# Optimization experiments

Measured on AMD Instinct MI355X. Metric: run time of the kernel, lower is better.

## Reference

```python
import jax, jax.numpy as jnp
import numpy as np

B, V, H, NT, K_CD = 4096, 1024, 1024, 2, 10
L1_REG, L2_REG = 1e-5, 1e-4


def setup_inputs() -> dict:
    key = jax.random.key(0)
    ks = jax.random.split(key, 10)
    v0 = jax.random.bernoulli(ks[0], 0.5, (B, V)).astype(jnp.float32)
    # two distinct non-trivial (non-Z) sites per sample, one in each half
    tau0 = jax.random.randint(ks[1], (B,), 0, V // 2)
    tau1 = V // 2 + jax.random.randint(ks[2], (B,), 0, V // 2)
    tau_idx = jnp.stack([tau0, tau1], axis=1).astype(jnp.int32)
    basis_choice = jax.random.randint(ks[3], (B, NT), 1, 3).astype(jnp.int32)  # X=1 or Y=2
    basis_ids = jnp.zeros((B, V), jnp.int32)
    basis_ids = basis_ids.at[jnp.arange(B)[:, None], tau_idx].set(basis_choice)
    s = 1.0 / np.sqrt(2.0)
    un = np.zeros((3, 2, 2, 2), np.float32)  # [basis, row, col, re/im]
    un[0, :, :, 0] = np.eye(2)                              # Z: identity
    un[1, :, :, 0] = s * np.array([[1, 1], [1, -1]])        # X: Hadamard
    un[2, :, :, 0] = s * np.array([[1, 0], [1, 0]])         # Y: K gate, real
    un[2, :, :, 1] = s * np.array([[0, -1], [0, 1]])        # Y: K gate, imag
    unitaries = jnp.asarray(un)
    weights_amp = jax.random.normal(ks[4], (H, V), jnp.float32) / np.sqrt(V)
    weights_phase = 0.01 * jax.random.normal(ks[5], (H, V), jnp.float32)
    visible_bias_amp = 0.01 * jax.random.normal(ks[6], (V,), jnp.float32)
    hidden_bias_amp = 0.01 * jax.random.normal(ks[7], (H,), jnp.float32)
    visible_bias_phase = 0.01 * jax.random.normal(ks[8], (V,), jnp.float32)
    hidden_bias_phase = 0.01 * jax.random.normal(ks[9], (H,), jnp.float32)
    return {"v0": v0, "basis_ids": basis_ids, "tau_idx": tau_idx, "unitaries": unitaries,
            "weights_amp": weights_amp, "visible_bias_amp": visible_bias_amp,
            "hidden_bias_amp": hidden_bias_amp, "weights_phase": weights_phase,
            "visible_bias_phase": visible_bias_phase, "hidden_bias_phase": hidden_bias_phase,
            "k": K_CD}


def _forward(v0, unitaries, weights_amp, visible_bias_amp, hidden_bias_amp,
             weights_phase, visible_bias_phase, hidden_bias_phase,
             basis_ids, tau_idx, k):
    Bsz, Vn = v0.shape
    NTn = tau_idx.shape[1]
    C = 2 ** NTn
    # all 2^NT assignments of the rotated (tau) sites -> [C, NT]
    S = jnp.asarray(np.array([[(c >> (NTn - 1 - t)) & 1 for t in range(NTn)]
                              for c in range(C)], np.int32))
    U = (unitaries[..., 0] + 1j * unitaries[..., 1]).astype(jnp.complex64)  # [3,2,2]
    b_tau = jnp.take_along_axis(basis_ids, tau_idx, axis=1)                 # [B,NT]
    v0_tau = jnp.take_along_axis(v0, tau_idx, axis=1).astype(jnp.int32)     # [B,NT]
    # product over tau sites of unitary elements U_b[v0_j, s_j] -> [B,C]
    Uelem = U[b_tau[:, None, :], v0_tau[:, None, :], S[None, :, :]]
    wU = jnp.prod(Uelem, axis=-1)
    # v' = v0 with tau sites replaced by each assignment s -> [B,C,V]
    onehot = jax.nn.one_hot(tau_idx, Vn, dtype=v0.dtype)                    # [B,NT,V]
    mask = onehot.sum(1)
    vp = v0[:, None, :] * (1.0 - mask[:, None, :]) \
         + jnp.einsum('btv,ct->bcv', onehot, S.astype(v0.dtype))
    # unnormalized wavefunction psi(v') = sqrt(p_amp(v')) * exp(i*log(p_phase(v'))/2)
    pre_amp = jnp.einsum('bcv,hv->bch', vp, weights_amp) + hidden_bias_amp
    pre_ph = jnp.einsum('bcv,hv->bch', vp, weights_phase) + hidden_bias_phase
    log_amp = 0.5 * (vp @ visible_bias_amp + jax.nn.softplus(pre_amp).sum(-1))  # [B,C]
    theta = 0.5 * (vp @ visible_bias_phase + jax.nn.softplus(pre_ph).sum(-1))
    # per-sample shift cancels exactly in A/B; keeps exp() in fp32 range
    log_amp = log_amp - jax.lax.stop_gradient(log_amp.max(axis=1, keepdims=True))
    psi = (jnp.exp(log_amp) * (jnp.cos(theta) + 1j * jnp.sin(theta))).astype(jnp.complex64)
    w = wU * psi                                   # [B,C] complex
    coef = w / w.sum(axis=1, keepdims=True)        # A/B weighting per sample
    sig_amp = jax.nn.sigmoid(pre_amp)
    sig_ph = jax.nn.sigmoid(pre_ph)
    inv_b = 1.0 / Bsz
    Lw_amp = jnp.einsum('bc,bch,bcv->hv', coef, sig_amp, vp) * inv_b
    Lw_ph = jnp.einsum('bc,bch,bcv->hv', coef, sig_ph, vp) * inv_b
    Lvb = jnp.einsum('bc,bcv->v', coef, vp) * inv_b
    Lhb_amp = jnp.einsum('bc,bch->h', coef, sig_amp) * inv_b
    Lhb_ph = jnp.einsum('bc,bch->h', coef, sig_ph) * inv_b
    # amplitude params take Re(L) (negated positive phase); phase params take Im(L)
    g_w_amp = -jnp.real(Lw_amp)
    g_vb_amp = -jnp.real(Lvb)
    g_hb_amp = -jnp.real(Lhb_amp)
    g_w_ph = jnp.imag(Lw_ph)
    g_vb_ph = jnp.imag(Lvb)
    g_hb_ph = jnp.imag(Lhb_ph)
    # ---- CD-k Gibbs negative phase (amplitude RBM only) ----
    base_key = jax.random.key(1234)
    def gibbs_step(i, v):
        kh = jax.random.fold_in(base_key, 2 * i)
        kv = jax.random.fold_in(base_key, 2 * i + 1)
        ph = jax.nn.sigmoid(v @ weights_amp.T + hidden_bias_amp)
        h = (jax.random.uniform(kh, ph.shape) < ph).astype(v.dtype)
        pv = jax.nn.sigmoid(h @ weights_amp + visible_bias_amp)
        return (jax.random.uniform(kv, pv.shape) < pv).astype(v.dtype)
    vk = jax.lax.stop_gradient(jax.lax.fori_loop(0, k, gibbs_step, v0))
    sig_k = jax.nn.sigmoid(vk @ weights_amp.T + hidden_bias_amp)
    g_w_amp = g_w_amp + jnp.einsum('bh,bv->hv', sig_k, vk) * inv_b
    g_vb_amp = g_vb_amp + vk.mean(0)
    g_hb_amp = g_hb_amp + sig_k.mean(0)
    # ---- L1/L2 regularization on weight gradients ----
    g_w_amp = g_w_amp + L2_REG * weights_amp + L1_REG * jnp.sign(weights_amp)
    g_w_ph = g_w_ph + L2_REG * weights_phase + L1_REG * jnp.sign(weights_phase)
    return (g_w_amp, g_vb_amp, g_hb_amp, g_w_ph, g_vb_ph, g_hb_ph)


def reference(v0, basis_ids, tau_idx, unitaries, weights_amp, visible_bias_amp,
              hidden_bias_amp, weights_phase, visible_bias_phase, hidden_bias_phase, k):
    return _forward(v0, unitaries, weights_amp, visible_bias_amp, hidden_bias_amp,
                    weights_phase, visible_bias_phase, hidden_bias_phase,
                    basis_ids, tau_idx, k)
```

## Files before the change

### kernel.cpp

```cpp
#include <hip/hip_runtime.h>
#include <cstdint>
#include <cstddef>

#define BSZ 4096
#define VN  1024
#define HN  1024
#define NSTEPS 10

static constexpr float INVB = 1.0f / 4096.0f;
static constexpr float L1R  = 1e-5f;
static constexpr float L2R  = 1e-4f;

typedef __attribute__((ext_vector_type(8)))  __bf16        bf16x8;
typedef __attribute__((ext_vector_type(8)))  unsigned short ushort8;
typedef __attribute__((ext_vector_type(16))) float          f32x16;

__device__ static inline unsigned short f2bf(float x){
  unsigned u = __float_as_uint(x);
  unsigned r = (u + 0x7FFFu + ((u >> 16) & 1u)) >> 16;
  return (unsigned short)r;
}
__device__ static inline float bf2f(unsigned short s){
  return __uint_as_float(((unsigned)s) << 16);
}

__device__ __forceinline__ void gload16(const void* g, void* l){
  __builtin_amdgcn_global_load_lds(
      (__attribute__((address_space(1))) void*)(g),
      (__attribute__((address_space(3))) void*)(l),
      16, 0, 0);
}

#define TFR(x0,x1,r) { x0 += x1; x1 = ((x1)<<(r))|((x1)>>(32-(r))); x1 ^= x0; }

__host__ __device__ static inline void tf2x32(unsigned k0, unsigned k1,
                                              unsigned x0, unsigned x1,
                                              unsigned &o0, unsigned &o1)
{
  const unsigned ks2 = k0 ^ k1 ^ 0x1BD11BDAu;
  x0 += k0; x1 += k1;
  TFR(x0,x1,13) TFR(x0,x1,15) TFR(x0,x1,26) TFR(x0,x1,6)
  x0 += k1; x1 += ks2 + 1u;
  TFR(x0,x1,17) TFR(x0,x1,29) TFR(x0,x1,16) TFR(x0,x1,24)
  x0 += ks2; x1 += k0 + 2u;
  TFR(x0,x1,13) TFR(x0,x1,15) TFR(x0,x1,26) TFR(x0,x1,6)
  x0 += k0; x1 += k1 + 3u;
  TFR(x0,x1,17) TFR(x0,x1,29) TFR(x0,x1,16) TFR(x0,x1,24)
  x0 += k1; x1 += ks2 + 4u;
  TFR(x0,x1,13) TFR(x0,x1,15) TFR(x0,x1,26) TFR(x0,x1,6)
  x0 += ks2; x1 += k0 + 5u;
  o0 = x0; o1 = x1;
}

__device__ static inline float tf_uniform(unsigned k0, unsigned k1, unsigned e)
{
  unsigned o0, o1; tf2x32(k0, k1, 0u, e, o0, o1);
  const unsigned r = o0 ^ o1;
  return __uint_as_float((r >> 9) | 0x3f800000u) - 1.0f;
}

__device__ static inline float sigmoidf(float x){ return 1.0f/(1.0f+expf(-x)); }
__device__ static inline float softplusf(float x){
  return fmaxf(x, 0.0f) + log1pf(expf(-fabsf(x)));
}

__global__ void zero_kernel(float* __restrict__ p, int n){
  int i = blockIdx.x*256 + threadIdx.x;
  if (i < n) p[i] = 0.0f;
}

__global__ void prep_kernel(const float* __restrict__ v0,
                            const int* __restrict__ tau,
                            float* __restrict__ v0m,
                            float* __restrict__ v_cur,
                            unsigned short* __restrict__ v0m_bf,
                            unsigned short* __restrict__ v_bf)
{
  int i = blockIdx.x*256 + threadIdx.x;
  int b = i >> 10;
  int v = i & (VN-1);
  float x = v0[i];
  v_cur[i] = x;
  v_bf[i]  = f2bf(x);
  int t0 = tau[2*b], t1 = tau[2*b+1];
  float xm = (v==t0 || v==t1) ? 0.0f : x;
  v0m[i]    = xm;
  v0m_bf[i] = f2bf(xm);
}

__global__ void transpose_kernel(const float* __restrict__ Wa,
                                 const float* __restrict__ Wp,
                                 float* __restrict__ WTa,
                                 float* __restrict__ WTp)
{
  __shared__ float tile[32][33];
  const float* in = blockIdx.z ? Wp : Wa;
  float* out      = blockIdx.z ? WTp : WTa;
  int x  = blockIdx.x*32 + threadIdx.x;
  int y0 = blockIdx.y*32;
  for (int j = threadIdx.y; j < 32; j += 8)
    tile[j][threadIdx.x] = in[(size_t)(y0+j)*VN + x];
  __syncthreads();
  int xo  = y0 + threadIdx.x;
  int yo0 = blockIdx.x*32;
  for (int j = threadIdx.y; j < 32; j += 8)
    out[(size_t)(yo0+j)*HN + xo] = tile[threadIdx.x][j];
}

__global__ void transpose_to_bf(const float* __restrict__ X,
                                unsigned short* __restrict__ XT)
{
  __shared__ float tile[32][33];
  int x  = blockIdx.x*32 + threadIdx.x;
  int y0 = blockIdx.y*32;
  for (int j = threadIdx.y; j < 32; j += 8)
    tile[j][threadIdx.x] = X[(size_t)(y0+j)*1024 + x];
  __syncthreads();
  int xo  = y0 + threadIdx.x;
  int yo0 = blockIdx.x*32;
  for (int j = threadIdx.y; j < 32; j += 8)
    XT[(size_t)(yo0+j)*BSZ + xo] = f2bf(tile[threadIdx.x][j]);
}

__global__ void split_weights(const float* __restrict__ Wa,
                              const float* __restrict__ Wp,
                              const float* __restrict__ WTa,
                              unsigned short* __restrict__ WaHi,
                              unsigned short* __restrict__ WaLo,
                              unsigned short* __restrict__ WpHi,
                              unsigned short* __restrict__ WpLo,
                              unsigned short* __restrict__ WaTHi,
                              unsigned short* __restrict__ WaTLo)
{
  size_t i = (size_t)blockIdx.x*256 + threadIdx.x;
  float w = Wa[i];  unsigned short h = f2bf(w);
  WaHi[i] = h;  WaLo[i] = f2bf(w - bf2f(h));
  w = Wp[i];  h = f2bf(w);
  WpHi[i] = h;  WpLo[i] = f2bf(w - bf2f(h));
  w = WTa[i]; h = f2bf(w);
  WaTHi[i] = h; WaTLo[i] = f2bf(w - bf2f(h));
}

#define GM 128
#define GN 64
#define GK 64

template<int MODE>
__global__ __launch_bounds__(256) void mfma_nt(
    const unsigned short* __restrict__ A,
    const unsigned short* __restrict__ Bhi,
    const unsigned short* __restrict__ Blo,
    const float* __restrict__ bias,
    unsigned short* __restrict__ out_bf,
    float* __restrict__ out_f,
    unsigned key0, unsigned key1)
{
  constexpr int K = 1024;
  constexpr int N = 1024;
  __shared__ ushort8 ldsA [GM*8];
  __shared__ ushort8 ldsBh[GN*8];
  __shared__ ushort8 ldsBl[GN*8];

  const int tid  = threadIdx.x;
  const int m0   = blockIdx.y*GM, n0 = blockIdx.x*GN;
  const int lane = tid & 63, w = tid >> 6;
  const int wm = w >> 1, wn = w & 1;
  const int l31 = lane & 31, hi = lane >> 5;

  const int rsub = lane >> 3;
  const int cch  = lane & 7;

  f32x16 acc0 = {}, acc1 = {};

  const int arow0 = wm*64 + l31;
  const int brow  = wn*32 + l31;
  const int aidx0 = arow0*8, aidx1 = (arow0+32)*8;
  const int bidx  = brow*8;
  const int aswz  = arow0 & 7;
  const int bswz  = brow & 7;

  for (int kt = 0; kt < K/GK; ++kt){
    __syncthreads();
    const size_t kbase = (size_t)kt*GK;
    #pragma unroll
    for (int p = 0; p < 4; p++){
      const int row  = p*32 + w*8 + rsub;
      const int csrc = cch ^ (row & 7);
      gload16(A + (size_t)(m0+row)*K + kbase + csrc*8,
              &ldsA[(p*32 + w*8)*8]);
    }
    #pragma unroll
    for (int p = 0; p < 2; p++){
      const int row  = p*32 + w*8 + rsub;
      const int csrc = cch ^ (row & 7);
      gload16(Bhi + (size_t)(n0+row)*K + kbase + csrc*8,
              &ldsBh[(p*32 + w*8)*8]);
      gload16(Blo + (size_t)(n0+row)*K + kbase + csrc*8,
              &ldsBl[(p*32 + w*8)*8]);
    }
    __syncthreads();

    #pragma unroll
    for (int s = 0; s < 4; s++){
      const int c = s*2 + hi;
      const bf16x8 a0 = __builtin_bit_cast(bf16x8, ldsA [aidx0 + (c ^ aswz)]);
      const bf16x8 a1 = __builtin_bit_cast(bf16x8, ldsA [aidx1 + (c ^ aswz)]);
      const bf16x8 bh = __builtin_bit_cast(bf16x8, ldsBh[bidx  + (c ^ bswz)]);
      const bf16x8 bl = __builtin_bit_cast(bf16x8, ldsBl[bidx  + (c ^ bswz)]);
      acc0 = __builtin_amdgcn_mfma_f32_32x32x16_bf16(a0, bh, acc0, 0, 0, 0);
      acc0 = __builtin_amdgcn_mfma_f32_32x32x16_bf16(a0, bl, acc0, 0, 0, 0);
      acc1 = __builtin_amdgcn_mfma_f32_32x32x16_bf16(a1, bh, acc1, 0, 0, 0);
      acc1 = __builtin_amdgcn_mfma_f32_32x32x16_bf16(a1, bl, acc1, 0, 0, 0);
    }
  }

  const int n  = n0 + wn*32 + l31;
  const float bv = bias[n];
  #pragma unroll
  for (int mt = 0; mt < 2; mt++){
    const f32x16 acc = mt ? acc1 : acc0;
    const int mbase = m0 + wm*64 + mt*32 + 4*hi;
    #pragma unroll
    for (int r = 0; r < 16; r++){
      const int m = mbase + (r&3) + 8*(r>>2);
      const float pre = acc[r] + bv;
      const size_t o = (size_t)m*N + n;
      if constexpr (MODE == 0 || MODE == 1){
        const float p = sigmoidf(pre);
        const float u = tf_uniform(key0, key1, (unsigned)(m*N + n));
        const float smp = (u < p) ? 1.0f : 0.0f;
        out_bf[o] = (u < p) ? (unsigned short)0x3F80 : (unsigned short)0;
        if constexpr (MODE == 1) out_f[o] = smp;
      } else if constexpr (MODE == 2){
        out_f[o] = sigmoidf(pre);
      } else {
        out_f[o] = pre;
      }
    }
  }
}

template<int NPROD>
__global__ __launch_bounds__(256) void mfma_grad(
    const unsigned short* __restrict__ A1,
    const unsigned short* __restrict__ B1,
    const unsigned short* __restrict__ A2,
    const unsigned short* __restrict__ B2,
    const float* __restrict__ Wreg,
    float* __restrict__ gW)
{
  constexpr int K = BSZ;
  __shared__ ushort8 lA1[64*8];
  __shared__ ushort8 lB1[64*8];
  __shared__ ushort8 lA2[(NPROD==2)?64*8:1];
  __shared__ ushort8 lB2[(NPROD==2)?64*8:1];

  const int tid  = threadIdx.x;
  const int m0   = blockIdx.y*64, n0 = blockIdx.x*64;
  const int lane = tid & 63, w = tid >> 6;
  const int wm = w >> 1, wn = w & 1;
  const int l31 = lane & 31, hi = lane >> 5;
  const int srow = tid >> 3, sc = tid & 7;

  f32x16 acc1a = {}, acc1b = {}, acc2a = {}, acc2b = {};

  const int arow = wm*32 + l31;
  const int brow = wn*32 + l31;
  const int aswz = arow & 7, bswz = brow & 7;
  const int aidx = arow*8,  bidx = brow*8;

  for (int kt = 0; kt < K/64; ++kt){
    __syncthreads();
    const size_t kof = (size_t)kt*64 + sc*8;
    #pragma unroll
    for (int p = 0; p < 2; p++){
      const int row = p*32 + srow;
      const int c = sc ^ (row & 7);
      lA1[row*8 + c] = *(const ushort8*)(A1 + (size_t)(m0+row)*K + kof);
      lB1[row*8 + c] = *(const ushort8*)(B1 + (size_t)(n0+row)*K + kof);
      if constexpr (NPROD==2){
        lA2[row*8 + c] = *(const ushort8*)(A2 + (size_t)(m0+row)*K + kof);
        lB2[row*8 + c] = *(const ushort8*)(B2 + (size_t)(n0+row)*K + kof);
      }
    }
    __syncthreads();
    #pragma unroll
    for (int s = 0; s < 4; s++){
      const int c = s*2 + hi;
      const bf16x8 a1 = __builtin_bit_cast(bf16x8, lA1[aidx + (c ^ aswz)]);
      const bf16x8 b1 = __builtin_bit_cast(bf16x8, lB1[bidx + (c ^ bswz)]);
      if (s & 1) acc1b = __builtin_amdgcn_mfma_f32_32x32x16_bf16(a1, b1, acc1b, 0,0,0);
      else       acc1a = __builtin_amdgcn_mfma_f32_32x32x16_bf16(a1, b1, acc1a, 0,0,0);
      if constexpr (NPROD==2){
        const bf16x8 a2 = __builtin_bit_cast(bf16x8, lA2[aidx + (c ^ aswz)]);
        const bf16x8 b2 = __builtin_bit_cast(bf16x8, lB2[bidx + (c ^ bswz)]);
        if (s & 1) acc2b = __builtin_amdgcn_mfma_f32_32x32x16_bf16(a2, b2, acc2b, 0,0,0);
        else       acc2a = __builtin_amdgcn_mfma_f32_32x32x16_bf16(a2, b2, acc2a, 0,0,0);
      }
    }
  }

  const int n = n0 + wn*32 + l31;
  #pragma unroll
  for (int r = 0; r < 16; r++){
    const int m = m0 + wm*32 + 4*hi + (r&3) + 8*(r>>2);
    const size_t o = (size_t)m*VN + n;
    float val;
    if constexpr (NPROD==2)
      val = INVB*((acc1a[r]+acc1b[r]) - (acc2a[r]+acc2b[r]));
    else
      val = INVB*(acc1a[r]+acc1b[r]);
    const float wv = Wreg[o];
    const float sg = (wv>0.f)?1.f:((wv<0.f)?-1.f:0.f);
    gW[o] += val + L2R*wv + L1R*sg;
  }
}

__global__ __launch_bounds__(256) void coef_ramp_kernel(
    const float* __restrict__ pre0a, const float* __restrict__ pre0p,
    const float* __restrict__ WTa,   const float* __restrict__ WTp,
    const float* __restrict__ v0,
    const float* __restrict__ vbA,   const float* __restrict__ vbP,
    const int*   __restrict__ tau,   const int*   __restrict__ basis,
    const float* __restrict__ unit,
    float* __restrict__ coefRe, float* __restrict__ coefIm,
    float* __restrict__ tmpA,   float* __restrict__ tmpP,
    float* __restrict__ Ramp,   float* __restrict__ Iph)
{
  const int b = blockIdx.x;
  const int t = threadIdx.x;
  const int t0 = tau[2*b], t1 = tau[2*b+1];

  float d[6] = {0,0,0,0,0,0};
  float st_sa[4], st_sp[4], st_a0[4], st_a1[4], st_p0[4], st_p1[4];

  #pragma unroll
  for (int i = 0; i < 4; i++){
    const int h = t + i*256;
    const float pa = pre0a[(size_t)b*HN + h], pp = pre0p[(size_t)b*HN + h];
    const float a0 = WTa[(size_t)t0*HN + h], a1 = WTa[(size_t)t1*HN + h];
    const float p0 = WTp[(size_t)t0*HN + h], p1 = WTp[(size_t)t1*HN + h];
    const float sa  = sigmoidf(pa);
    const float sp  = sigmoidf(pp);
    const float s1a = sa*(1.f-sa), ta2 = 1.f-2.f*sa, s2a = s1a*ta2;
    const float s1p = sp*(1.f-sp), tp2 = 1.f-2.f*sp, s2p = s1p*tp2;
    const float a01 = a0 + a1, p01 = p0 + p1;
    d[0] += a1 *(sa + a1 *(0.5f*s1a + 0.16666667f*a1 *s2a));
    d[1] += a0 *(sa + a0 *(0.5f*s1a + 0.16666667f*a0 *s2a));
    d[2] += a01*(sa + a01*(0.5f*s1a + 0.16666667f*a01*s2a));
    d[3] += p1 *(sp + p1 *(0.5f*s1p + 0.16666667f*p1 *s2p));
    d[4] += p0 *(sp + p0 *(0.5f*s1p + 0.16666667f*p0 *s2p));
    d[5] += p01*(sp + p01*(0.5f*s1p + 0.16666667f*p01*s2p));
    st_sa[i]=sa; st_sp[i]=sp; st_a0[i]=a0; st_a1[i]=a1; st_p0[i]=p0; st_p1[i]=p1;
  }

  __shared__ float red[6][4];
  __shared__ float lcr[4], lci[4];
  const int lane = t & 63, wv = t >> 6;
  #pragma unroll
  for (int i=0;i<6;i++){
    float x = d[i];
    for (int off=32; off>0; off>>=1) x += __shfl_down(x, off);
    if (lane==0) red[i][wv] = x;
  }
  __syncthreads();

  if (t==0){
    double ds[6];
    #pragma unroll
    for (int i=0;i<6;i++)
      ds[i] = (double)red[i][0]+red[i][1]+red[i][2]+red[i][3];

    const int bas0 = basis[(size_t)b*VN + t0], bas1 = basis[(size_t)b*VN + t1];
    const int x0 = (int)v0[(size_t)b*VN + t0], x1 = (int)v0[(size_t)b*VN + t1];
    const double A0 = vbA[t0], A1 = vbA[t1], P0 = vbP[t0], P1 = vbP[t1];

    double la[4], th[4];
    la[0]=0.0;                th[0]=0.0;
    la[1]=0.5*(A1+ds[0]);     th[1]=0.5*(P1+ds[3]);
    la[2]=0.5*(A0+ds[1]);     th[2]=0.5*(P0+ds[4]);
    la[3]=0.5*(A0+A1+ds[2]);  th[3]=0.5*(P0+P1+ds[5]);

    double wR[4], wI[4], sr=0.0, si=0.0;
    #pragma unroll
    for (int c=0;c<4;c++){
      const int s0 = (c>>1)&1, s1 = c&1;
      const float* u0 = unit + (((size_t)bas0*2 + x0)*2 + s0)*2;
      const float* u1 = unit + (((size_t)bas1*2 + x1)*2 + s1)*2;
      const double uR = (double)u0[0]*u1[0] - (double)u0[1]*u1[1];
      const double uI = (double)u0[0]*u1[1] + (double)u0[1]*u1[0];
      const double e  = exp(la[c]);
      const double cs = cos(th[c]), sn = sin(th[c]);
      wR[c] = e*(uR*cs - uI*sn);
      wI[c] = e*(uR*sn + uI*cs);
      sr += wR[c]; si += wI[c];
    }
    const double dd = sr*sr + si*si;
    #pragma unroll
    for (int c=0;c<4;c++){
      const float cr = (float)((wR[c]*sr + wI[c]*si)/dd);
      const float ci = (float)((wI[c]*sr - wR[c]*si)/dd);
      coefRe[b*4+c] = cr;  coefIm[b*4+c] = ci;
      lcr[c] = cr;         lci[c] = ci;
    }
    atomicAdd(tmpA + t0, lcr[2]+lcr[3]);
    atomicAdd(tmpA + t1, lcr[1]+lcr[3]);
    atomicAdd(tmpP + t0, lci[2]+lci[3]);
    atomicAdd(tmpP + t1, lci[1]+lci[3]);
  }
  __syncthreads();

  const float cr0=lcr[0], cr1=lcr[1], cr2=lcr[2], cr3=lcr[3];
  const float ci0=lci[0], ci1=lci[1], ci2=lci[2], ci3=lci[3];

  #pragma unroll
  for (int i = 0; i < 4; i++){
    const int h = t + i*256;
    const float sa = st_sa[i], sp = st_sp[i];
    const float a0 = st_a0[i], a1 = st_a1[i], p0 = st_p0[i], p1 = st_p1[i];
    const float s1a = sa*(1.f-sa), ta2 = 1.f-2.f*sa;
    const float s2a = s1a*ta2,     s3a = s1a*(ta2*ta2 - 2.f*s1a);
    const float s1p = sp*(1.f-sp), tp2 = 1.f-2.f*sp;
    const float s2p = s1p*tp2,     s3p = s1p*(tp2*tp2 - 2.f*s1p);
    const float a01 = a0 + a1, p01 = p0 + p1;
    const float sgA1 = sa + a1 *(s1a + a1 *(0.5f*s2a + 0.16666667f*a1 *s3a));
    const float sgA0 = sa + a0 *(s1a + a0 *(0.5f*s2a + 0.16666667f*a0 *s3a));
    const float sgA01= sa + a01*(s1a + a01*(0.5f*s2a + 0.16666667f*a01*s3a));
    const float sgP1 = sp + p1 *(s1p + p1 *(0.5f*s2p + 0.16666667f*p1 *s3p));
    const float sgP0 = sp + p0 *(s1p + p0 *(0.5f*s2p + 0.16666667f*p0 *s3p));
    const float sgP01= sp + p01*(s1p + p01*(0.5f*s2p + 0.16666667f*p01*s3p));
    Ramp[(size_t)b*HN + h] = cr0*sa + cr1*sgA1 + cr2*sgA0 + cr3*sgA01;
    Iph [(size_t)b*HN + h] = ci0*sp + ci1*sgP1 + ci2*sgP0 + ci3*sgP01;
  }
}

__global__ void csr_count(const int* __restrict__ tau, int* __restrict__ cnt){
  int b = blockIdx.x*256 + threadIdx.x;
  atomicAdd(cnt + tau[2*b],   1);
  atomicAdd(cnt + tau[2*b+1], 1);
}

__global__ __launch_bounds__(1024) void csr_scan(const int* __restrict__ cnt,
                                                 int* __restrict__ off,
                                                 int* __restrict__ cur){
  __shared__ int s[1024];
  const int t = threadIdx.x;
  s[t] = cnt[t];
  __syncthreads();
  for (int d=1; d<1024; d<<=1){
    int v = 0;
    if (t >= d) v = s[t-d];
    __syncthreads();
    s[t] += v;
    __syncthreads();
  }
  const int excl = (t==0) ? 0 : s[t-1];
  off[t] = excl; cur[t] = excl;
}

__global__ void csr_fill(const int* __restrict__ tau, int* __restrict__ cur,
                         int* __restrict__ list){
  int b = blockIdx.x*256 + threadIdx.x;
  int p0 = atomicAdd(cur + tau[2*b],   1); list[p0] = b;
  int p1 = atomicAdd(cur + tau[2*b+1], 1); list[p1] = b;
}

__global__ __launch_bounds__(256) void scatter_v2(
    const float* __restrict__ pre0a, const float* __restrict__ pre0p,
    const float* __restrict__ WTa,   const float* __restrict__ WTp,
    const int*   __restrict__ tau,
    const float* __restrict__ coefRe, const float* __restrict__ coefIm,
    const int* __restrict__ cnt, const int* __restrict__ off,
    const int* __restrict__ list,
    float* __restrict__ gWa, float* __restrict__ gWp)
{
  const int v = blockIdx.x;
  const int n = cnt[v];
  if (n == 0) return;
  const int o = off[v];
  const int c_lo = (v < 512) ? 2 : 1;

  for (int hh = 0; hh < 2; hh++){
    const int h = blockIdx.y*512 + hh*256 + threadIdx.x;
    const float av = WTa[(size_t)v*HN + h];
    const float pv = WTp[(size_t)v*HN + h];
    float accA = 0.f, accP = 0.f;
    for (int e = o; e < o + n; e++){
      const int b = list[e];
      const int t0 = tau[2*b], t1 = tau[2*b+1];
      const int other = (v < 512) ? t1 : t0;
      const float aoA = WTa[(size_t)other*HN + h];
      const float aoP = WTp[(size_t)other*HN + h];
      const float pa  = pre0a[(size_t)b*HN + h];
      const float pp  = pre0p[(size_t)b*HN + h];
      const float crl = coefRe[b*4 + c_lo], cr3 = coefRe[b*4 + 3];
      const float cil = coefIm[b*4 + c_lo], ci3 = coefIm[b*4 + 3];
      accA += crl*sigmoidf(pa + av) + cr3*sigmoidf(pa + av + aoA);
      accP += cil*sigmoidf(pp + pv) + ci3*sigmoidf(pp + pv + aoP);
    }
    gWa[(size_t)h*VN + v] += -INVB*accA;
    gWp[(size_t)h*VN + v] +=  INVB*accP;
  }
}

__global__ __launch_bounds__(256) void colsum_v2(
    const float* __restrict__ v0m, const float* __restrict__ vk,
    const float* __restrict__ sigk, const float* __restrict__ Ramp,
    const float* __restrict__ Iph,
    float* __restrict__ csV0m, float* __restrict__ csVk,
    float* __restrict__ csSigk, float* __restrict__ csRamp,
    float* __restrict__ csIph)
{
  const int j  = blockIdx.x*256 + threadIdx.x;
  const int b0 = blockIdx.y*128;
  float s1=0,s2=0,s3=0,s4=0,s5=0;
  for (int b=b0; b<b0+128; b++){
    const size_t o = (size_t)b*1024 + j;
    s1 += v0m[o]; s2 += vk[o]; s3 += sigk[o]; s4 += Ramp[o]; s5 += Iph[o];
  }
  atomicAdd(csV0m+j, s1); atomicAdd(csVk+j, s2); atomicAdd(csSigk+j, s3);
  atomicAdd(csRamp+j, s4); atomicAdd(csIph+j, s5);
}

__global__ void final_small(
    const float* __restrict__ csV0m, const float* __restrict__ csVk,
    const float* __restrict__ csSigk, const float* __restrict__ csRamp,
    const float* __restrict__ csIph,
    const float* __restrict__ tmpA, const float* __restrict__ tmpP,
    float* __restrict__ gVa, float* __restrict__ gHa,
    float* __restrict__ gVp, float* __restrict__ gHp)
{
  const int j = blockIdx.x*256 + threadIdx.x;
  if (j < VN){
    gVa[j] = INVB*(csVk[j] - csV0m[j] - tmpA[j]);
    gVp[j] = INVB*tmpP[j];
  }
  if (j < HN){
    gHa[j] = INVB*(csSigk[j] - csRamp[j]);
    gHp[j] = INVB*csIph[j];
  }
}

extern "C" void kernel_launch(void* const* d_in, const int* in_sizes, int n_in,
                              void* d_out, int out_size, void* d_ws, size_t ws_size,
                              hipStream_t stream)
{
  const float* v0    = (const float*)d_in[0];
  const int*   basis = (const int*)  d_in[1];
  const int*   tau   = (const int*)  d_in[2];
  const float* unit  = (const float*)d_in[3];
  const float* Wa    = (const float*)d_in[4];
  const float* vbA   = (const float*)d_in[5];
  const float* hbA   = (const float*)d_in[6];
  const float* Wp    = (const float*)d_in[7];
  const float* vbP   = (const float*)d_in[8];
  const float* hbP   = (const float*)d_in[9];

  float* ws    = (float*)d_ws;
  float* v0m   = ws;  ws += (size_t)BSZ*VN;
  float* v_cur = ws;  ws += (size_t)BSZ*VN;
  float* h_buf = ws;  ws += (size_t)BSZ*HN;
  float* WTa   = ws;  ws += (size_t)VN*HN;
  float* WTp   = ws;  ws += (size_t)VN*HN;
  float* pre0a = ws;  ws += (size_t)BSZ*HN;
  float* pre0p = ws;  ws += (size_t)BSZ*HN;
  float* Ramp  = ws;  ws += (size_t)BSZ*HN;
  float* Iph   = ws;  ws += (size_t)BSZ*HN;
  float* coefRe= ws;  ws += (size_t)BSZ*4;
  float* coefIm= ws;  ws += (size_t)BSZ*4;
  float* tmpA  = ws;  ws += VN;
  float* tmpP  = ws;  ws += VN;
  float* csV0m = ws;  ws += VN;
  float* csVk  = ws;  ws += VN;
  float* csSigk= ws;  ws += HN;
  float* csRamp= ws;  ws += HN;
  float* csIph = ws;  ws += HN;
  int*   csrCnt = (int*)ws;  ws += VN;
  int*   csrOff = (int*)ws;  ws += VN;
  int*   csrCur = (int*)ws;  ws += VN;
  int*   csrLst = (int*)ws;  ws += 2*BSZ;
  unsigned short* v_bf    = (unsigned short*)ws;  ws += (size_t)BSZ*VN/2;
  unsigned short* h_bf    = (unsigned short*)ws;  ws += (size_t)BSZ*HN/2;
  unsigned short* v0m_bf  = (unsigned short*)ws;  ws += (size_t)BSZ*VN/2;
  unsigned short* WaHi    = (unsigned short*)ws;  ws += (size_t)HN*VN/2;
  unsigned short* WaLo    = (unsigned short*)ws;  ws += (size_t)HN*VN/2;
  unsigned short* WpHi    = (unsigned short*)ws;  ws += (size_t)HN*VN/2;
  unsigned short* WpLo    = (unsigned short*)ws;  ws += (size_t)HN*VN/2;
  unsigned short* WaTHi   = (unsigned short*)ws;  ws += (size_t)HN*VN/2;
  unsigned short* WaTLo   = (unsigned short*)ws;  ws += (size_t)HN*VN/2;

  float* sig_k = h_buf;
  unsigned short* v0mT  = (unsigned short*)pre0a;
  unsigned short* vkT   = v0mT + (size_t)VN*BSZ;
  unsigned short* RampT = (unsigned short*)pre0p;
  unsigned short* IphT  = RampT + (size_t)HN*BSZ;
  unsigned short* sigkT = (unsigned short*)WTa;

  float* out = (float*)d_out;
  float* gWa = out;
  float* gVa = gWa + (size_t)HN*VN;
  float* gHa = gVa + VN;
  float* gWp = gHa + HN;
  float* gVp = gWp + (size_t)HN*VN;
  float* gHp = gVp + VN;

  const dim3 gemm_grid(VN/GN, BSZ/GM);
  const dim3 tr_grid(1024/32, BSZ/32);
  const dim3 tr_blk(32, 8);

  zero_kernel<<<dim3(40), 256, 0, stream>>>(tmpA, 10*1024);
  zero_kernel<<<dim3((out_size+255)/256), 256, 0, stream>>>(out, out_size);
  prep_kernel<<<dim3(BSZ*VN/256), 256, 0, stream>>>(v0, tau, v0m, v_cur, v0m_bf, v_bf);
  transpose_kernel<<<dim3(VN/32, HN/32, 2), dim3(32,8), 0, stream>>>(Wa, Wp, WTa, WTp);
  split_weights<<<dim3(HN*VN/256), 256, 0, stream>>>(
      Wa, Wp, WTa, WaHi, WaLo, WpHi, WpLo, WaTHi, WaTLo);

  mfma_nt<3><<<gemm_grid, 256, 0, stream>>>(
      v0m_bf, WaHi, WaLo, hbA, nullptr, pre0a, 0u, 0u);
  mfma_nt<3><<<gemm_grid, 256, 0, stream>>>(
      v0m_bf, WpHi, WpLo, hbP, nullptr, pre0p, 0u, 0u);
  coef_ramp_kernel<<<dim3(BSZ), 256, 0, stream>>>(
      pre0a, pre0p, WTa, WTp, v0, vbA, vbP, tau, basis, unit,
      coefRe, coefIm, tmpA, tmpP, Ramp, Iph);

  csr_count<<<dim3(BSZ/256), 256, 0, stream>>>(tau, csrCnt);
  csr_scan <<<dim3(1), 1024, 0, stream>>>(csrCnt, csrOff, csrCur);
  csr_fill <<<dim3(BSZ/256), 256, 0, stream>>>(tau, csrCur, csrLst);
  scatter_v2<<<dim3(VN, 2), 256, 0, stream>>>(
      pre0a, pre0p, WTa, WTp, tau, coefRe, coefIm,
      csrCnt, csrOff, csrLst, gWa, gWp);

  for (int i = 0; i < NSTEPS; i++){
    unsigned kh0, kh1, kv0, kv1;
    tf2x32(0u, 1234u, 0u, (unsigned)(2*i),   kh0, kh1);
    tf2x32(0u, 1234u, 0u, (unsigned)(2*i+1), kv0, kv1);
    mfma_nt<0><<<gemm_grid, 256, 0, stream>>>(
        v_bf, WaHi, WaLo, hbA, h_bf, nullptr, kh0, kh1);
    mfma_nt<1><<<gemm_grid, 256, 0, stream>>>(
        h_bf, WaTHi, WaTLo, vbA, v_bf, v_cur, kv0, kv1);
  }
  mfma_nt<2><<<gemm_grid, 256, 0, stream>>>(
      v_bf, WaHi, WaLo, hbA, nullptr, sig_k, 0u, 0u);

  colsum_v2<<<dim3(4, 32), 256, 0, stream>>>(
      v0m, v_cur, sig_k, Ramp, Iph, csV0m, csVk, csSigk, csRamp, csIph);
  transpose_to_bf<<<tr_grid, tr_blk, 0, stream>>>(v0m,   v0mT);
  transpose_to_bf<<<tr_grid, tr_blk, 0, stream>>>(v_cur, vkT);
  transpose_to_bf<<<tr_grid, tr_blk, 0, stream>>>(Ramp,  RampT);
  transpose_to_bf<<<tr_grid, tr_blk, 0, stream>>>(Iph,   IphT);
  transpose_to_bf<<<tr_grid, tr_blk, 0, stream>>>(sig_k, sigkT);

  mfma_grad<2><<<dim3(VN/64, HN/64), 256, 0, stream>>>(
      sigkT, vkT, RampT, v0mT, Wa, gWa);
  mfma_grad<1><<<dim3(VN/64, HN/64), 256, 0, stream>>>(
      IphT, v0mT, nullptr, nullptr, Wp, gWp);

  final_small<<<dim3(4), 256, 0, stream>>>(
      csV0m, csVk, csSigk, csRamp, csIph, tmpA, tmpP, gVa, gHa, gVp, gHp);
}
```

Measured before the change: 1.029 ms.

## Fuse Gibbs chain into one cooperative persistent kernel with double-buffered LDS

Replaces the 21 separate GEMM launches of the Gibbs sampling chain with a single cooperative kernel that loops over steps, using grid.sync between dependent half-steps. The inner K loop now double-buffers LDS tiles so global loads for the next tile overlap the MFMA work on the current one. This aims to remove per-launch overhead and load latency stalls. It relies on all 512 blocks being co-resident, which is why launch bounds allow two blocks per CU, and it falls back to the old launch sequence if the cooperative launch fails. Grid-wide barriers add their own synchronisation cost.

```diff
diff --git a/kernel.cpp b/kernel.cpp
--- a/kernel.cpp
+++ b/kernel.cpp
@@ -1,6 +1,9 @@
 #include <hip/hip_runtime.h>
+#include <hip/hip_cooperative_groups.h>
 #include <cstdint>
 #include <cstddef>
+
+namespace cg = cooperative_groups;
 
 #define BSZ 4096
 #define VN  1024
@@ -14,6 +17,8 @@
 typedef __attribute__((ext_vector_type(8)))  __bf16        bf16x8;
 typedef __attribute__((ext_vector_type(8)))  unsigned short ushort8;
 typedef __attribute__((ext_vector_type(16))) float          f32x16;
+
+struct GibbsKeys { unsigned k[21][2]; };
 
 __device__ static inline unsigned short f2bf(float x){
   unsigned u = __float_as_uint(x);
@@ -60,9 +65,6 @@
 }
 
 __device__ static inline float sigmoidf(float x){ return 1.0f/(1.0f+expf(-x)); }
-__device__ static inline float softplusf(float x){
-  return fmaxf(x, 0.0f) + log1pf(expf(-fabsf(x)));
-}
 
 __global__ void zero_kernel(float* __restrict__ p, int n){
   int i = blockIdx.x*256 + threadIdx.x;
@@ -166,7 +168,6 @@
   const int lane = tid & 63, w = tid >> 6;
   const int wm = w >> 1, wn = w & 1;
   const int l31 = lane & 31, hi = lane >> 5;
-
   const int rsub = lane >> 3;
   const int cch  = lane & 7;
 
@@ -186,17 +187,14 @@
     for (int p = 0; p < 4; p++){
       const int row  = p*32 + w*8 + rsub;
       const int csrc = cch ^ (row & 7);
-      gload16(A + (size_t)(m0+row)*K + kbase + csrc*8,
-              &ldsA[(p*32 + w*8)*8]);
+      gload16(A + (size_t)(m0+row)*K + kbase + csrc*8, &ldsA[(p*32 + w*8)*8]);
     }
     #pragma unroll
     for (int p = 0; p < 2; p++){
       const int row  = p*32 + w*8 + rsub;
       const int csrc = cch ^ (row & 7);
-      gload16(Bhi + (size_t)(n0+row)*K + kbase + csrc*8,
-              &ldsBh[(p*32 + w*8)*8]);
-      gload16(Blo + (size_t)(n0+row)*K + kbase + csrc*8,
-              &ldsBl[(p*32 + w*8)*8]);
+      gload16(Bhi + (size_t)(n0+row)*K + kbase + csrc*8, &ldsBh[(p*32 + w*8)*8]);
+      gload16(Blo + (size_t)(n0+row)*K + kbase + csrc*8, &ldsBl[(p*32 + w*8)*8]);
     }
     __syncthreads();
 
@@ -228,14 +226,154 @@
       if constexpr (MODE == 0 || MODE == 1){
         const float p = sigmoidf(pre);
         const float u = tf_uniform(key0, key1, (unsigned)(m*N + n));
-        const float smp = (u < p) ? 1.0f : 0.0f;
         out_bf[o] = (u < p) ? (unsigned short)0x3F80 : (unsigned short)0;
-        if constexpr (MODE == 1) out_f[o] = smp;
+        if constexpr (MODE == 1) out_f[o] = (u < p) ? 1.0f : 0.0f;
       } else if constexpr (MODE == 2){
         out_f[o] = sigmoidf(pre);
       } else {
         out_f[o] = pre;
       }
+    }
+  }
+}
+
+__global__ __launch_bounds__(256, 2) void gibbs_chain(
+    unsigned short* __restrict__ v_bf,
+    unsigned short* __restrict__ h_bf,
+    const unsigned short* __restrict__ WaHi,
+    const unsigned short* __restrict__ WaLo,
+    const unsigned short* __restrict__ WaTHi,
+    const unsigned short* __restrict__ WaTLo,
+    const float* __restrict__ hbA,
+    const float* __restrict__ vbA,
+    float* __restrict__ v_cur,
+    float* __restrict__ sig_k,
+    GibbsKeys keys)
+{
+  constexpr int K = 1024;
+  constexpr int N = 1024;
+  __shared__ ushort8 ldsA [2][GM*8];
+  __shared__ ushort8 ldsBh[2][GN*8];
+  __shared__ ushort8 ldsBl[2][GN*8];
+
+  cg::grid_group grid = cg::this_grid();
+
+  const int bid  = blockIdx.x;
+  const int bx   = bid & 15, by = bid >> 4;
+  const int m0   = by*GM, n0 = bx*GN;
+  const int tid  = threadIdx.x;
+  const int lane = tid & 63, w = tid >> 6;
+  const int wm = w >> 1, wn = w & 1;
+  const int l31 = lane & 31, hi = lane >> 5;
+  const int rsub = lane >> 3;
+  const int cch  = lane & 7;
+
+  const int arow0 = wm*64 + l31;
+  const int brow  = wn*32 + l31;
+  const int aidx0 = arow0*8, aidx1 = (arow0+32)*8;
+  const int bidx  = brow*8;
+  const int aswz  = arow0 & 7;
+  const int bswz  = brow & 7;
+  const int n     = n0 + wn*32 + l31;
+
+  #pragma unroll 1
+  for (int s = 0; s < 21; ++s){
+    const bool hdir = ((s & 1) == 0);
+    const unsigned short* A  = hdir ? v_bf : h_bf;
+    const unsigned short* Bh = hdir ? WaHi : WaTHi;
+    const unsigned short* Bl = hdir ? WaLo : WaTLo;
+    const float* bias        = hdir ? hbA : vbA;
+
+    f32x16 acc0 = {}, acc1 = {};
+
+    {
+      #pragma unroll
+      for (int p = 0; p < 4; p++){
+        const int row  = p*32 + w*8 + rsub;
+        const int csrc = cch ^ (row & 7);
+        gload16(A + (size_t)(m0+row)*K + csrc*8, &ldsA[0][(p*32 + w*8)*8]);
+      }
+      #pragma unroll
+      for (int p = 0; p < 2; p++){
+        const int row  = p*32 + w*8 + rsub;
+        const int csrc = cch ^ (row & 7);
+        gload16(Bh + (size_t)(n0+row)*K + csrc*8, &ldsBh[0][(p*32 + w*8)*8]);
+        gload16(Bl + (size_t)(n0+row)*K + csrc*8, &ldsBl[0][(p*32 + w*8)*8]);
+      }
+    }
+
+    #pragma unroll 2
+    for (int kt = 0; kt < K/GK; ++kt){
+      const int cur = kt & 1;
+      if (kt + 1 < K/GK){
+        const size_t kbase = (size_t)(kt+1)*GK;
+        #pragma unroll
+        for (int p = 0; p < 4; p++){
+          const int row  = p*32 + w*8 + rsub;
+          const int csrc = cch ^ (row & 7);
+          gload16(A + (size_t)(m0+row)*K + kbase + csrc*8,
+                  &ldsA[cur^1][(p*32 + w*8)*8]);
+        }
+        #pragma unroll
+        for (int p = 0; p < 2; p++){
+          const int row  = p*32 + w*8 + rsub;
+          const int csrc = cch ^ (row & 7);
+          gload16(Bh + (size_t)(n0+row)*K + kbase + csrc*8,
+                  &ldsBh[cur^1][(p*32 + w*8)*8]);
+          gload16(Bl + (size_t)(n0+row)*K + kbase + csrc*8,
+                  &ldsBl[cur^1][(p*32 + w*8)*8]);
+        }
+        asm volatile("s_waitcnt vmcnt(8)" ::: "memory");
+      } else {
+        asm volatile("s_waitcnt vmcnt(0)" ::: "memory");
+      }
+      __builtin_amdgcn_sched_barrier(0);
+      __builtin_amdgcn_s_barrier();
+      __builtin_amdgcn_sched_barrier(0);
+
+      #pragma unroll
+      for (int sf = 0; sf < 4; sf++){
+        const int c = sf*2 + hi;
+        const bf16x8 a0 = __builtin_bit_cast(bf16x8, ldsA [cur][aidx0 + (c ^ aswz)]);
+        const bf16x8 a1 = __builtin_bit_cast(bf16x8, ldsA [cur][aidx1 + (c ^ aswz)]);
+        const bf16x8 bh = __builtin_bit_cast(bf16x8, ldsBh[cur][bidx  + (c ^ bswz)]);
+        const bf16x8 bl = __builtin_bit_cast(bf16x8, ldsBl[cur][bidx  + (c ^ bswz)]);
+        acc0 = __builtin_amdgcn_mfma_f32_32x32x16_bf16(a0, bh, acc0, 0, 0, 0);
+        acc0 = __builtin_amdgcn_mfma_f32_32x32x16_bf16(a0, bl, acc0, 0, 0, 0);
+        acc1 = __builtin_amdgcn_mfma_f32_32x32x16_bf16(a1, bh, acc1, 0, 0, 0);
+        acc1 = __builtin_amdgcn_mfma_f32_32x32x16_bf16(a1, bl, acc1, 0, 0, 0);
+      }
+      __builtin_amdgcn_sched_barrier(0);
+      __builtin_amdgcn_s_barrier();
+      __builtin_amdgcn_sched_barrier(0);
+    }
+
+    const float bv = bias[n];
+    const unsigned k0 = keys.k[s][0], k1 = keys.k[s][1];
+    unsigned short* outb = hdir ? h_bf : v_bf;
+    #pragma unroll
+    for (int mt = 0; mt < 2; mt++){
+      const f32x16 acc = mt ? acc1 : acc0;
+      const int mbase = m0 + wm*64 + mt*32 + 4*hi;
+      #pragma unroll
+      for (int r = 0; r < 16; r++){
+        const int m = mbase + (r&3) + 8*(r>>2);
+        const float pre = acc[r] + bv;
+        const size_t o = (size_t)m*N + n;
+        if (s == 20){
+          sig_k[o] = sigmoidf(pre);
+        } else {
+          const float p = sigmoidf(pre);
+          const float u = tf_uniform(k0, k1, (unsigned)(m*N + n));
+          outb[o] = (u < p) ? (unsigned short)0x3F80 : (unsigned short)0;
+          if (s == 19) v_cur[o] = (u < p) ? 1.0f : 0.0f;
+        }
+      }
+    }
+
+    if (s < 20){
+      __threadfence();
+      grid.sync();
     }
   }
 }
@@ -630,17 +768,30 @@
       pre0a, pre0p, WTa, WTp, tau, coefRe, coefIm,
       csrCnt, csrOff, csrLst, gWa, gWp);
 
+  GibbsKeys hk;
   for (int i = 0; i < NSTEPS; i++){
-    unsigned kh0, kh1, kv0, kv1;
-    tf2x32(0u, 1234u, 0u, (unsigned)(2*i),   kh0, kh1);
-    tf2x32(0u, 1234u, 0u, (unsigned)(2*i+1), kv0, kv1);
-    mfma_nt<0><<<gemm_grid, 256, 0, stream>>>(
-        v_bf, WaHi, WaLo, hbA, h_bf, nullptr, kh0, kh1);
-    mfma_nt<1><<<gemm_grid, 256, 0, stream>>>(
-        h_bf, WaTHi, WaTLo, vbA, v_bf, v_cur, kv0, kv1);
-  }
-  mfma_nt<2><<<gemm_grid, 256, 0, stream>>>(
-      v_bf, WaHi, WaLo, hbA, nullptr, sig_k, 0u, 0u);
+    tf2x32(0u, 1234u, 0u, (unsigned)(2*i),   hk.k[2*i][0],   hk.k[2*i][1]);
+    tf2x32(0u, 1234u, 0u, (unsigned)(2*i+1), hk.k[2*i+1][0], hk.k[2*i+1][1]);
+  }
+  hk.k[20][0] = 0u; hk.k[20][1] = 0u;
+
+  void* cargs[] = {
+    (void*)&v_bf, (void*)&h_bf, (void*)&WaHi, (void*)&WaLo,
+    (void*)&WaTHi, (void*)&WaTLo, (void*)&hbA, (void*)&vbA,
+    (void*)&v_cur, (void*)&sig_k, (void*)&hk
+  };
+  hipError_t cerr = hipLaunchCooperativeKernel(
+      (void*)gibbs_chain, dim3(512), dim3(256), cargs, 0, stream);
+  if (cerr != hipSuccess){
+    for (int i = 0; i < NSTEPS; i++){
+      mfma_nt<0><<<gemm_grid, 256, 0, stream>>>(
+          v_bf, WaHi, WaLo, hbA, h_bf, nullptr, hk.k[2*i][0], hk.k[2*i][1]);
+      mfma_nt<1><<<gemm_grid, 256, 0, stream>>>(
+          h_bf, WaTHi, WaTLo, vbA, v_bf, v_cur, hk.k[2*i+1][0], hk.k[2*i+1][1]);
+    }
+    mfma_nt<2><<<gemm_grid, 256, 0, stream>>>(
+        v_bf, WaHi, WaLo, hbA, nullptr, sig_k, 0u, 0u);
+  }
 
   colsum_v2<<<dim3(4, 32), 256, 0, stream>>>(
       v0m, v_cur, sig_k, Ramp, Iph, csV0m, csVk, csSigk, csRamp, csIph);
```

Measured after the change: 3.034 ms. 2.95x slower.

## Shrink GEMM M-tile, swizzle block order, split scatter wider, skip intermediate fp32 writes

Applied to the files above, without the earlier changes.

Shrinks the mfma_nt tile from 128x64 to 64x64, so each wave now holds one accumulator instead of two. Block indices are remapped with a stride-8 swizzle, presumably to improve L2 locality or spread work across XCDs. scatter_v2 gets twice as many blocks, each covering 256 h values instead of 512, for more parallelism. The Gibbs loop also stops writing the fp32 visible sample on every step except the last, which cuts global stores. The trade-off is that smaller tiles reload B once per 64 rows, raising global and LDS traffic relative to MFMA work, and the swizzle assumes a 16x64 grid.

```diff
diff --git a/kernel.cpp b/kernel.cpp
--- a/kernel.cpp
+++ b/kernel.cpp
@@ -60,9 +60,6 @@
 }
 
 __device__ static inline float sigmoidf(float x){ return 1.0f/(1.0f+expf(-x)); }
-__device__ static inline float softplusf(float x){
-  return fmaxf(x, 0.0f) + log1pf(expf(-fabsf(x)));
-}
 
 __global__ void zero_kernel(float* __restrict__ p, int n){
   int i = blockIdx.x*256 + threadIdx.x;
@@ -141,7 +138,7 @@
   WaTHi[i] = h; WaTLo[i] = f2bf(w - bf2f(h));
 }
 
-#define GM 128
+#define GM 64
 #define GN 64
 #define GK 64
 
@@ -161,81 +158,68 @@
   __shared__ ushort8 ldsBh[GN*8];
   __shared__ ushort8 ldsBl[GN*8];
 
+  const int orig = blockIdx.x + gridDim.x * blockIdx.y;
+  const int swz  = (orig & 7) * 128 + (orig >> 3);
+  const int bx   = swz & 15, by = swz >> 4;
+  const int m0   = by*GM, n0 = bx*GN;
+
   const int tid  = threadIdx.x;
-  const int m0   = blockIdx.y*GM, n0 = blockIdx.x*GN;
   const int lane = tid & 63, w = tid >> 6;
   const int wm = w >> 1, wn = w & 1;
   const int l31 = lane & 31, hi = lane >> 5;
-
   const int rsub = lane >> 3;
   const int cch  = lane & 7;
 
-  f32x16 acc0 = {}, acc1 = {};
-
-  const int arow0 = wm*64 + l31;
-  const int brow  = wn*32 + l31;
-  const int aidx0 = arow0*8, aidx1 = (arow0+32)*8;
-  const int bidx  = brow*8;
-  const int aswz  = arow0 & 7;
-  const int bswz  = brow & 7;
+  f32x16 acc = {};
+
+  const int arow = wm*32 + l31;
+  const int brow = wn*32 + l31;
+  const int aswz = arow & 7;
+  const int bswz = brow & 7;
+  const int aidx = arow*8;
+  const int bidx = brow*8;
 
   for (int kt = 0; kt < K/GK; ++kt){
     __syncthreads();
     const size_t kbase = (size_t)kt*GK;
     #pragma unroll
-    for (int p = 0; p < 4; p++){
-      const int row  = p*32 + w*8 + rsub;
-      const int csrc = cch ^ (row & 7);
-      gload16(A + (size_t)(m0+row)*K + kbase + csrc*8,
-              &ldsA[(p*32 + w*8)*8]);
-    }
-    #pragma unroll
     for (int p = 0; p < 2; p++){
       const int row  = p*32 + w*8 + rsub;
       const int csrc = cch ^ (row & 7);
-      gload16(Bhi + (size_t)(n0+row)*K + kbase + csrc*8,
-              &ldsBh[(p*32 + w*8)*8]);
-      gload16(Blo + (size_t)(n0+row)*K + kbase + csrc*8,
-              &ldsBl[(p*32 + w*8)*8]);
+      gload16(A   + (size_t)(m0+row)*K + kbase + csrc*8, &ldsA [(p*32 + w*8)*8]);
+      gload16(Bhi + (size_t)(n0+row)*K + kbase + csrc*8, &ldsBh[(p*32 + w*8)*8]);
+      gload16(Blo + (size_t)(n0+row)*K + kbase + csrc*8, &ldsBl[(p*32 + w*8)*8]);
     }
     __syncthreads();
 
     #pragma unroll
     for (int s = 0; s < 4; s++){
       const int c = s*2 + hi;
-      const bf16x8 a0 = __builtin_bit_cast(bf16x8, ldsA [aidx0 + (c ^ aswz)]);
-      const bf16x8 a1 = __builtin_bit_cast(bf16x8, ldsA [aidx1 + (c ^ aswz)]);
-      const bf16x8 bh = __builtin_bit_cast(bf16x8, ldsBh[bidx  + (c ^ bswz)]);
-      const bf16x8 bl = __builtin_bit_cast(bf16x8, ldsBl[bidx  + (c ^ bswz)]);
-      acc0 = __builtin_amdgcn_mfma_f32_32x32x16_bf16(a0, bh, acc0, 0, 0, 0);
-      acc0 = __builtin_amdgcn_mfma_f32_32x32x16_bf16(a0, bl, acc0, 0, 0, 0);
-      acc1 = __builtin_amdgcn_mfma_f32_32x32x16_bf16(a1, bh, acc1, 0, 0, 0);
-      acc1 = __builtin_amdgcn_mfma_f32_32x32x16_bf16(a1, bl, acc1, 0, 0, 0);
+      const bf16x8 a  = __builtin_bit_cast(bf16x8, ldsA [aidx + (c ^ aswz)]);
+      const bf16x8 bh = __builtin_bit_cast(bf16x8, ldsBh[bidx + (c ^ bswz)]);
+      const bf16x8 bl = __builtin_bit_cast(bf16x8, ldsBl[bidx + (c ^ bswz)]);
+      acc = __builtin_amdgcn_mfma_f32_32x32x16_bf16(a, bh, acc, 0, 0, 0);
+      acc = __builtin_amdgcn_mfma_f32_32x32x16_bf16(a, bl, acc, 0, 0, 0);
     }
   }
 
   const int n  = n0 + wn*32 + l31;
   const float bv = bias[n];
+  const int mbase = m0 + wm*32 + 4*hi;
   #pragma unroll
-  for (int mt = 0; mt < 2; mt++){
-    const f32x16 acc = mt ? acc1 : acc0;
-    const int mbase = m0 + wm*64 + mt*32 + 4*hi;
-    #pragma unroll
-    for (int r = 0; r < 16; r++){
-      const int m = mbase + (r&3) + 8*(r>>2);
-      const float pre = acc[r] + bv;
-      const size_t o = (size_t)m*N + n;
-      if constexpr (MODE == 0 || MODE == 1){
-        const float p = sigmoidf(pre);
-        const float u = tf_uniform(key0, key1, (unsigned)(m*N + n));
-        const float smp = (u < p) ? 1.0f : 0.0f;
-        out_bf[o] = (u < p) ? (unsigned short)0x3F80 : (unsigned short)0;
-        if constexpr (MODE == 1) out_f[o] = smp;
-      } else if constexpr (MODE == 2){
-        out_f[o] = sigmoidf(pre);
-      } else {
-        out_f[o] = pre;
-      }
+  for (int r = 0; r < 16; r++){
+    const int m = mbase + (r&3) + 8*(r>>2);
+    const float pre = acc[r] + bv;
+    const size_t o = (size_t)m*N + n;
+    if constexpr (MODE == 0 || MODE == 1){
+      const float p = sigmoidf(pre);
+      const float u = tf_uniform(key0, key1, (unsigned)(m*N + n));
+      out_bf[o] = (u < p) ? (unsigned short)0x3F80 : (unsigned short)0;
+      if constexpr (MODE == 1) out_f[o] = (u < p) ? 1.0f : 0.0f;
+    } else if constexpr (MODE == 2){
+      out_f[o] = sigmoidf(pre);
+    } else {
+      out_f[o] = pre;
     }
   }
 }
@@ -480,27 +464,25 @@
   const int o = off[v];
   const int c_lo = (v < 512) ? 2 : 1;
 
-  for (int hh = 0; hh < 2; hh++){
-    const int h = blockIdx.y*512 + hh*256 + threadIdx.x;
-    const float av = WTa[(size_t)v*HN + h];
-    const float pv = WTp[(size_t)v*HN + h];
-    float accA = 0.f, accP = 0.f;
-    for (int e = o; e < o + n; e++){
-      const int b = list[e];
-      const int t0 = tau[2*b], t1 = tau[2*b+1];
-      const int other = (v < 512) ? t1 : t0;
-      const float aoA = WTa[(size_t)other*HN + h];
-      const float aoP = WTp[(size_t)other*HN + h];
-      const float pa  = pre0a[(size_t)b*HN + h];
-      const float pp  = pre0p[(size_t)b*HN + h];
-      const float crl = coefRe[b*4 + c_lo], cr3 = coefRe[b*4 + 3];
-      const float cil = coefIm[b*4 + c_lo], ci3 = coefIm[b*4 + 3];
-      accA += crl*sigmoidf(pa + av) + cr3*sigmoidf(pa + av + aoA);
-      accP += cil*sigmoidf(pp + pv) + ci3*sigmoidf(pp + pv + aoP);
-    }
-    gWa[(size_t)h*VN + v] += -INVB*accA;
-    gWp[(size_t)h*VN + v] +=  INVB*accP;
-  }
+  const int h = blockIdx.y*256 + threadIdx.x;
+  const float av = WTa[(size_t)v*HN + h];
+  const float pv = WTp[(size_t)v*HN + h];
+  float accA = 0.f, accP = 0.f;
+  for (int e = o; e < o + n; e++){
+    const int b = list[e];
+    const int t0 = tau[2*b], t1 = tau[2*b+1];
+    const int other = (v < 512) ? t1 : t0;
+    const float aoA = WTa[(size_t)other*HN + h];
+    const float aoP = WTp[(size_t)other*HN + h];
+    const float pa  = pre0a[(size_t)b*HN + h];
+    const float pp  = pre0p[(size_t)b*HN + h];
+    const float crl = coefRe[b*4 + c_lo], cr3 = coefRe[b*4 + 3];
+    const float cil = coefIm[b*4 + c_lo], ci3 = coefIm[b*4 + 3];
+    accA += crl*sigmoidf(pa + av) + cr3*sigmoidf(pa + av + aoA);
+    accP += cil*sigmoidf(pp + pv) + ci3*sigmoidf(pp + pv + aoP);
+  }
+  gWa[(size_t)h*VN + v] += -INVB*accA;
+  gWp[(size_t)h*VN + v] +=  INVB*accP;
 }
 
 __global__ __launch_bounds__(256) void colsum_v2(
@@ -626,7 +608,7 @@
   csr_count<<<dim3(BSZ/256), 256, 0, stream>>>(tau, csrCnt);
   csr_scan <<<dim3(1), 1024, 0, stream>>>(csrCnt, csrOff, csrCur);
   csr_fill <<<dim3(BSZ/256), 256, 0, stream>>>(tau, csrCur, csrLst);
-  scatter_v2<<<dim3(VN, 2), 256, 0, stream>>>(
+  scatter_v2<<<dim3(VN, 4), 256, 0, stream>>>(
       pre0a, pre0p, WTa, WTp, tau, coefRe, coefIm,
       csrCnt, csrOff, csrLst, gWa, gWp);
 
@@ -636,8 +618,12 @@
     tf2x32(0u, 1234u, 0u, (unsigned)(2*i+1), kv0, kv1);
     mfma_nt<0><<<gemm_grid, 256, 0, stream>>>(
         v_bf, WaHi, WaLo, hbA, h_bf, nullptr, kh0, kh1);
-    mfma_nt<1><<<gemm_grid, 256, 0, stream>>>(
-        h_bf, WaTHi, WaTLo, vbA, v_bf, v_cur, kv0, kv1);
+    if (i < NSTEPS-1)
+      mfma_nt<0><<<gemm_grid, 256, 0, stream>>>(
+          h_bf, WaTHi, WaTLo, vbA, v_bf, nullptr, kv0, kv1);
+    else
+      mfma_nt<1><<<gemm_grid, 256, 0, stream>>>(
+          h_bf, WaTHi, WaTLo, vbA, v_bf, v_cur, kv0, kv1);
   }
   mfma_nt<2><<<gemm_grid, 256, 0, stream>>>(
       v_bf, WaHi, WaLo, hbA, nullptr, sig_k, 0u, 0u);
```

Result: faster. 987.1 us (-4.1%).
